# Kernel tuning notes

Hardware: AMD Instinct MI355X
Metric: run time of the kernel (lower is better)

The kernel has to match this reference:

```python
import jax, jax.numpy as jnp
import numpy as np

N = 200_000      # nodes
E = 6_400_000    # edges (avg degree 32)
IN = 128         # in_channels
H = 16           # GCN/GRU hidden size (fixed by module)
OUT = 32         # out_channels


def setup_inputs() -> dict:
    key = jax.random.key(0)
    ks = jax.random.split(key, 13)
    s = 0.1  # weight init scale
    return {
        "x": jax.random.normal(ks[0], (N, IN), jnp.float32),
        "edge_index": jax.random.randint(ks[1], (2, E), 0, N, dtype=jnp.int32),
        "batch": jnp.zeros((N,), jnp.int32),
        "W1": jax.random.normal(ks[2], (IN, H), jnp.float32) * s,
        "b1": jax.random.normal(ks[3], (H,), jnp.float32) * s,
        "W2": jax.random.normal(ks[4], (H, H), jnp.float32) * s,
        "b2": jax.random.normal(ks[5], (H,), jnp.float32) * s,
        # GRU params, torch layout: [3H, in] stacked (r, z, n)
        "w_ih": jax.random.normal(ks[6], (3 * H, H), jnp.float32) * s,
        "w_hh": jax.random.normal(ks[7], (3 * H, H), jnp.float32) * s,
        "b_ih": jax.random.normal(ks[8], (3 * H,), jnp.float32) * s,
        "b_hh": jax.random.normal(ks[9], (3 * H,), jnp.float32) * s,
        # final Linear
        "Wfc": jax.random.normal(ks[10], (OUT, H), jnp.float32) * s,
        "bfc": jax.random.normal(ks[11], (OUT,), jnp.float32) * s,
    }


def gcn_conv(x, edge_index, W, b):
    """PyG GCNConv: transform, then sym-normalized aggregate with self-loops."""
    n = x.shape[0]
    h = x @ W                                   # [N, H]
    src, dst = edge_index[0], edge_index[1]
    # degree with self-loops: 1 + in-degree at target nodes
    deg = jax.ops.segment_sum(jnp.ones_like(dst, jnp.float32), dst, num_segments=n) + 1.0
    dinv = jax.lax.rsqrt(deg)                   # [N]
    norm = dinv[src] * dinv[dst]                # [E]
    agg = jax.ops.segment_sum(h[src] * norm[:, None], dst, num_segments=n)
    # self-loop message: h[i] * dinv[i]^2
    agg = agg + h * (dinv * dinv)[:, None]
    return agg + b


def reference(x, edge_index, batch, W1, b1, W2, b2, w_ih, w_hh, b_ih, b_hh, Wfc, bfc):
    h = jax.nn.relu(gcn_conv(x, edge_index, W1, b1))
    h = jax.nn.relu(gcn_conv(h, edge_index, W2, b2))
    # x.view(batch.size(0), -1, 16) -> [N, 1, 16]: GRU with seq_len=1, h0=0
    n_nodes = batch.shape[0]
    h0 = jnp.zeros((n_nodes, H), h.dtype)
    gi = h @ w_ih.T + b_ih                      # [N, 3H]
    gh = h0 @ w_hh.T + b_hh                     # [N, 3H]
    i_r, i_z, i_n = jnp.split(gi, 3, axis=1)
    h_r, h_z, h_n = jnp.split(gh, 3, axis=1)
    r = jax.nn.sigmoid(i_r + h_r)
    z = jax.nn.sigmoid(i_z + h_z)
    n_ = jnp.tanh(i_n + r * h_n)
    hseq = (1.0 - z) * n_ + z * h0              # last (only) timestep output
    return hseq @ Wfc.T + bfc                   # [N, OUT]
```

## Files before the change

### kernel.cpp

```cpp
#include <hip/hip_runtime.h>
#include <hip/hip_fp16.h>
#include <math.h>

#define HC 16
#define INC 128
#define OUTC 32
#define BKT_SHIFT 8
#define CAP 9216
#define NBMAX 1024
#define BINS 12512

typedef _Float16 f16;
typedef _Float16 f16x8 __attribute__((ext_vector_type(8)));


__global__ void init_gcur_kernel(int* __restrict__ gcur, int nbkt) {
    int i = blockIdx.x * blockDim.x + threadIdx.x;
    if (i < nbkt) gcur[i] = i * CAP;
}

__global__ void __launch_bounds__(512) bin_kernel(
        const int* __restrict__ src, const int* __restrict__ dst,
        int* __restrict__ gcur, int* __restrict__ csrbuf, int e, int nbkt) {
    __shared__ int ent[BINS];
    __shared__ int hist[NBMAX];
    __shared__ int off[NBMAX];
    __shared__ int gbase[NBMAX];
    __shared__ int wsum[8];
    int tid = threadIdx.x;
    int beg = blockIdx.x * BINS;
    int end = min(beg + BINS, e);
    int sz = end - beg;
    if (sz <= 0) return;

    for (int i = tid; i < NBMAX; i += 512) hist[i] = 0;
    __syncthreads();
    for (int i = beg + tid; i < end; i += 512)
        atomicAdd(&hist[dst[i] >> BKT_SHIFT], 1);
    __syncthreads();
    int b0 = tid * 2;
    int c0 = hist[b0], c1 = hist[b0 + 1];
    int tsum = c0 + c1;
    int lane = tid & 63, wid = tid >> 6;
    int v = tsum;
#pragma unroll
    for (int d = 1; d < 64; d <<= 1) {
        int u = __shfl_up(v, d, 64);
        if (lane >= d) v += u;
    }
    if (lane == 63) wsum[wid] = v;
    __syncthreads();
    int wbase = 0;
#pragma unroll
    for (int w = 0; w < 8; ++w) wbase += (w < wid) ? wsum[w] : 0;
    int ex = wbase + v - tsum;
    off[b0]     = ex;
    off[b0 + 1] = ex + c0;
    if (c0) gbase[b0]     = atomicAdd(&gcur[b0], c0);
    if (c1) gbase[b0 + 1] = atomicAdd(&gcur[b0 + 1], c1);
    hist[b0] = 0; hist[b0 + 1] = 0;
    __syncthreads();
    for (int i = beg + tid; i < end; i += 512) {
        int d = dst[i];
        int b = d >> BKT_SHIFT;
        int p = off[b] + atomicAdd(&hist[b], 1);
        ent[p] = (src[i] & 0x3FFFF) | ((d & 255) << 18);
    }
    __syncthreads();
    for (int k0 = 0; k0 < sz; k0 += 512) {
        int k = k0 + tid;
        if (k < sz) {
            int lo = 0, hi = nbkt - 1;
            while (lo < hi) {
                int mid = (lo + hi + 1) >> 1;
                if (off[mid] <= k) lo = mid; else hi = mid - 1;
            }
            csrbuf[gbase[lo] + (k - off[lo])] = ent[k];
        }
    }
}

__global__ void __launch_bounds__(512) bucketize_kernel(
        const int* __restrict__ gcur, int* __restrict__ csrbuf,
        int* __restrict__ row_beg, int* __restrict__ row_end,
        float* __restrict__ dinv, int n) {
    __shared__ int ent[CAP];
    __shared__ int cnt[256];
    __shared__ int off[256];
    __shared__ int cur[256];
    int tid = threadIdx.x;
    int b = blockIdx.x;
    int base = b * CAP;
    int sz = gcur[b] - base;
    if (sz > CAP) sz = CAP;
    int node0 = b << BKT_SHIFT;
    int nnodes = min(256, n - node0);
    for (int i = tid; i < sz; i += 512) ent[i] = csrbuf[base + i];
    if (tid < 256) cnt[tid] = 0;
    __syncthreads();
    for (int i = tid; i < sz; i += 512) atomicAdd(&cnt[ent[i] >> 18], 1);
    __syncthreads();
    int v = (tid < 256) ? cnt[tid] : 0;
    if (tid < 256) off[tid] = v;
    __syncthreads();
    for (int d = 1; d < 256; d <<= 1) {
        int u = (tid < 256 && tid >= d) ? off[tid - d] : 0;
        __syncthreads();
        if (tid < 256) off[tid] += u;
        __syncthreads();
    }
    if (tid < 256) {
        int excl = off[tid] - v;
        cur[tid] = excl;
        if (tid < nnodes) {
            row_beg[node0 + tid] = base + excl;
            row_end[node0 + tid] = base + excl + v;
            dinv[node0 + tid] = rsqrtf((float)v + 1.0f);
        }
    }
    __syncthreads();
    for (int i = tid; i < sz; i += 512) {
        int p = ent[i];
        int dl = p >> 18;
        int pos = atomicAdd(&cur[dl], 1);
        csrbuf[base + pos] = p & 0x3FFFF;
    }
}

__global__ void gemm1_kernel(const float* __restrict__ x, const float* __restrict__ W1,
                             const float* __restrict__ dinv, f16* __restrict__ hd1, int n) {
    __shared__ float sW[INC * HC];
    for (int i = threadIdx.x; i < INC * HC; i += blockDim.x) sW[i] = W1[i];
    __syncthreads();
    int node = blockIdx.x * blockDim.x + threadIdx.x;
    if (node >= n) return;
    const float4* xr = (const float4*)(x + (size_t)node * INC);
    float acc[HC];
#pragma unroll
    for (int f = 0; f < HC; ++f) acc[f] = 0.f;
#pragma unroll 4
    for (int k4 = 0; k4 < INC / 4; ++k4) {
        float4 v = xr[k4];
        const float* w = &sW[k4 * 4 * HC];
#pragma unroll
        for (int f = 0; f < HC; ++f)
            acc[f] += v.x * w[f] + v.y * w[HC + f] + v.z * w[2 * HC + f] + v.w * w[3 * HC + f];
    }
    float di = dinv[node];
    union { f16 h[HC]; float4 q[2]; } u;
#pragma unroll
    for (int f = 0; f < HC; ++f) u.h[f] = (f16)(acc[f] * di);
    float4* hl = (float4*)(hd1 + (size_t)node * HC);
    hl[0] = u.q[0];
    hl[1] = u.q[1];
}

__device__ __forceinline__ float gather_row16(
        const f16* __restrict__ hd, const int* __restrict__ csr,
        int beg, int end, int node, int f) {
    int h = f & 1;
    int k = f >> 1;
    float a0 = 0.f, a1 = 0.f, a2 = 0.f, a3 = 0.f;
    float a4 = 0.f, a5 = 0.f, a6 = 0.f, a7 = 0.f;
    int jj = beg + k;
    if (jj < end) {
        int s = csr[jj];
        jj += 8;
        for (; jj < end; jj += 8) {
            int sn = csr[jj];
            f16x8 v = *(const f16x8*)(hd + ((size_t)s << 4) + (h << 3));
            a0 += (float)v[0]; a1 += (float)v[1]; a2 += (float)v[2]; a3 += (float)v[3];
            a4 += (float)v[4]; a5 += (float)v[5]; a6 += (float)v[6]; a7 += (float)v[7];
            s = sn;
        }
        f16x8 v = *(const f16x8*)(hd + ((size_t)s << 4) + (h << 3));
        a0 += (float)v[0]; a1 += (float)v[1]; a2 += (float)v[2]; a3 += (float)v[3];
        a4 += (float)v[4]; a5 += (float)v[5]; a6 += (float)v[6]; a7 += (float)v[7];
    }
#pragma unroll
    for (int m = 2; m <= 8; m <<= 1) {
        a0 += __shfl_xor(a0, m, 16); a1 += __shfl_xor(a1, m, 16);
        a2 += __shfl_xor(a2, m, 16); a3 += __shfl_xor(a3, m, 16);
        a4 += __shfl_xor(a4, m, 16); a5 += __shfl_xor(a5, m, 16);
        a6 += __shfl_xor(a6, m, 16); a7 += __shfl_xor(a7, m, 16);
    }
    float e = a0;
    e = (k == 1) ? a1 : e;
    e = (k == 2) ? a2 : e;
    e = (k == 3) ? a3 : e;
    e = (k == 4) ? a4 : e;
    e = (k == 5) ? a5 : e;
    e = (k == 6) ? a6 : e;
    e = (k == 7) ? a7 : e;
    float gsum = __shfl(e, ((f & 7) << 1) | (f >> 3), 16);
    return gsum + (float)hd[(size_t)node * HC + f];
}

__global__ void __launch_bounds__(256) gather_fuse1_kernel(
        const f16* __restrict__ hd1, const int* __restrict__ csr,
        const int* __restrict__ row_beg, const int* __restrict__ row_end,
        const float* __restrict__ dinv, const float* __restrict__ b1,
        const float* __restrict__ W2, f16* __restrict__ hd2, int n) {
    __shared__ float sW[HC * 17];
    __shared__ float sb[HC];
    if (threadIdx.x < HC * HC) sW[(threadIdx.x >> 4) * 17 + (threadIdx.x & 15)] = W2[threadIdx.x];
    if (threadIdx.x < HC) sb[threadIdx.x] = b1[threadIdx.x];
    __syncthreads();
    int t = blockIdx.x * blockDim.x + threadIdx.x;
    int node = t >> 4;
    if (node >= n) return;
    int f = t & 15;
    float acc = gather_row16(hd1, csr, row_beg[node], row_end[node], node, f);
    float di = dinv[node];
    float h1 = fmaxf(acc * di + sb[f], 0.f);
    float a2 = 0.f;
#pragma unroll
    for (int k = 0; k < HC; ++k) {
        float hk = __shfl(h1, k, 16);
        a2 += hk * sW[k * 17 + f];
    }
    hd2[(size_t)node * HC + f] = (f16)(a2 * di);
}

__global__ void __launch_bounds__(256) gather_final_kernel(
        const f16* __restrict__ hd2, const int* __restrict__ csr,
        const int* __restrict__ row_beg, const int* __restrict__ row_end,
        const float* __restrict__ dinv, const float* __restrict__ b2,
        const float* __restrict__ w_ih, const float* __restrict__ b_ih,
        const float* __restrict__ b_hh, const float* __restrict__ Wfc,
        const float* __restrict__ bfc, float* __restrict__ out, int n) {
    __shared__ float s_wih[3 * HC * 17];
    __shared__ float s_wfc[OUTC * 17];
    __shared__ float s_bih[3 * HC], s_bhh[3 * HC], s_bfc[OUTC], s_b2[HC];
    for (int i = threadIdx.x; i < 3 * HC * HC; i += 256)
        s_wih[(i >> 4) * 17 + (i & 15)] = w_ih[i];
    for (int i = threadIdx.x; i < OUTC * HC; i += 256)
        s_wfc[(i >> 4) * 17 + (i & 15)] = Wfc[i];
    if (threadIdx.x < 3 * HC) { s_bih[threadIdx.x] = b_ih[threadIdx.x]; s_bhh[threadIdx.x] = b_hh[threadIdx.x]; }
    if (threadIdx.x < OUTC) s_bfc[threadIdx.x] = bfc[threadIdx.x];
    if (threadIdx.x < HC) s_b2[threadIdx.x] = b2[threadIdx.x];
    __syncthreads();
    int t = blockIdx.x * blockDim.x + threadIdx.x;
    int node = t >> 4;
    if (node >= n) return;
    int f = t & 15;
    float acc = gather_row16(hd2, csr, row_beg[node], row_end[node], node, f);
    float h = fmaxf(acc * dinv[node] + s_b2[f], 0.f);
    float ir = s_bih[f], iz = s_bih[HC + f], inn = s_bih[2 * HC + f];
#pragma unroll
    for (int k = 0; k < HC; ++k) {
        float hk = __shfl(h, k, 16);
        ir  += hk * s_wih[f * 17 + k];
        iz  += hk * s_wih[(HC + f) * 17 + k];
        inn += hk * s_wih[(2 * HC + f) * 17 + k];
    }
    float r = 1.f / (1.f + __expf(-(ir + s_bhh[f])));
    float z = 1.f / (1.f + __expf(-(iz + s_bhh[HC + f])));
    float nn = tanhf(inn + r * s_bhh[2 * HC + f]);
    float hs = (1.f - z) * nn;
    float a1 = s_bfc[f], a2 = s_bfc[HC + f];
#pragma unroll
    for (int k = 0; k < HC; ++k) {
        float hk = __shfl(hs, k, 16);
        a1 += hk * s_wfc[f * 17 + k];
        a2 += hk * s_wfc[(HC + f) * 17 + k];
    }
    float* orow = out + (size_t)node * OUTC;
    __builtin_nontemporal_store(a1, orow + f);
    __builtin_nontemporal_store(a2, orow + HC + f);
}

extern "C" void kernel_launch(void* const* d_in, const int* in_sizes, int n_in,
                              void* d_out, int out_size, void* d_ws, size_t ws_size,
                              hipStream_t stream) {
    const float* x     = (const float*)d_in[0];
    const int*   ei    = (const int*)d_in[1];
    const float* W1    = (const float*)d_in[3];
    const float* b1    = (const float*)d_in[4];
    const float* W2    = (const float*)d_in[5];
    const float* b2    = (const float*)d_in[6];
    const float* w_ih  = (const float*)d_in[7];
    const float* b_ih  = (const float*)d_in[9];
    const float* b_hh  = (const float*)d_in[10];
    const float* Wfc   = (const float*)d_in[11];
    const float* bfc   = (const float*)d_in[12];
    float* out = (float*)d_out;

    const int n = in_sizes[2];
    const int e = in_sizes[1] / 2;
    const int* src = ei;
    const int* dst = ei + e;
    const int nbkt = (n + 255) >> BKT_SHIFT;

    int*   gcur    = (int*)d_ws;
    int*   row_beg = gcur + 1024;
    int*   row_end = row_beg + n;
    float* dinv    = (float*)(row_end + n);
    int*   csrbuf  = (int*)(dinv + n);
    f16*   hd1     = (f16*)(csrbuf + (size_t)nbkt * CAP);
    f16*   hd2     = hd1 + (size_t)n * HC;

    const int B = 256;
    int gn   = (n + B - 1) / B;
    int gnf  = (int)(((long long)n * HC + B - 1) / B);
    int gbin = (e + BINS - 1) / BINS;

    init_gcur_kernel<<<(NBMAX + B - 1) / B, B, 0, stream>>>(gcur, nbkt);
    bin_kernel<<<gbin, 512, 0, stream>>>(src, dst, gcur, csrbuf, e, nbkt);
    bucketize_kernel<<<nbkt, 512, 0, stream>>>(gcur, csrbuf, row_beg, row_end, dinv, n);

    gemm1_kernel<<<gn, B, 0, stream>>>(x, W1, dinv, hd1, n);
    gather_fuse1_kernel<<<gnf, B, 0, stream>>>(hd1, csrbuf, row_beg, row_end, dinv, b1, W2, hd2, n);
    gather_final_kernel<<<gnf, B, 0, stream>>>(hd2, csrbuf, row_beg, row_end, dinv, b2,
                                               w_ih, b_ih, b_hh, Wfc, bfc, out, n);
}
```

Measured before the change: 458.9 us.

## Cache edges in registers, copy bins per bucket, shuffle-scan in bucketize

New measurement: 448.2 us. 1.02x faster.

```diff
diff --git a/kernel.cpp b/kernel.cpp
--- a/kernel.cpp
+++ b/kernel.cpp
@@ -8,7 +8,8 @@
 #define BKT_SHIFT 8
 #define CAP 9216
 #define NBMAX 1024
-#define BINS 12512
+#define BINS 12288
+#define EPT 24
 
 typedef _Float16 f16;
 typedef _Float16 f16x8 __attribute__((ext_vector_type(8)));
@@ -30,14 +31,22 @@
     int tid = threadIdx.x;
     int beg = blockIdx.x * BINS;
     int end = min(beg + BINS, e);
-    int sz = end - beg;
-    if (sz <= 0) return;
-
+    if (end <= beg) return;
+
+    int myd[EPT], mys[EPT];
+#pragma unroll
+    for (int u = 0; u < EPT; ++u) {
+        int i = beg + u * 512 + tid;
+        myd[u] = (i < end) ? dst[i] : -1;
+        mys[u] = (i < end) ? src[i] : 0;
+    }
     for (int i = tid; i < NBMAX; i += 512) hist[i] = 0;
     __syncthreads();
-    for (int i = beg + tid; i < end; i += 512)
-        atomicAdd(&hist[dst[i] >> BKT_SHIFT], 1);
-    __syncthreads();
+#pragma unroll
+    for (int u = 0; u < EPT; ++u)
+        if (myd[u] >= 0) atomicAdd(&hist[myd[u] >> BKT_SHIFT], 1);
+    __syncthreads();
+
     int b0 = tid * 2;
     int c0 = hist[b0], c1 = hist[b0 + 1];
     int tsum = c0 + c1;
@@ -60,23 +69,27 @@
     if (c1) gbase[b0 + 1] = atomicAdd(&gcur[b0 + 1], c1);
     hist[b0] = 0; hist[b0 + 1] = 0;
     __syncthreads();
-    for (int i = beg + tid; i < end; i += 512) {
-        int d = dst[i];
-        int b = d >> BKT_SHIFT;
-        int p = off[b] + atomicAdd(&hist[b], 1);
-        ent[p] = (src[i] & 0x3FFFF) | ((d & 255) << 18);
-    }
-    __syncthreads();
-    for (int k0 = 0; k0 < sz; k0 += 512) {
-        int k = k0 + tid;
-        if (k < sz) {
-            int lo = 0, hi = nbkt - 1;
-            while (lo < hi) {
-                int mid = (lo + hi + 1) >> 1;
-                if (off[mid] <= k) lo = mid; else hi = mid - 1;
-            }
-            csrbuf[gbase[lo] + (k - off[lo])] = ent[k];
+
+#pragma unroll
+    for (int u = 0; u < EPT; ++u) {
+        int d = myd[u];
+        if (d >= 0) {
+            int b = d >> BKT_SHIFT;
+            int p = off[b] + atomicAdd(&hist[b], 1);
+            ent[p] = (mys[u] & 0x3FFFF) | ((d & 255) << 18);
         }
+    }
+    __syncthreads();
+
+    int grp = tid >> 4;
+    int gl  = tid & 15;
+    for (int b = grp; b < nbkt; b += 32) {
+        int o = off[b];
+        int c = off[b + 1] - o;
+        if (c <= 0) continue;
+        int g = gbase[b];
+        for (int k = gl; k < c; k += 16)
+            csrbuf[g + k] = ent[o + k];
     }
 }
 
@@ -88,6 +101,7 @@
     __shared__ int cnt[256];
     __shared__ int off[256];
     __shared__ int cur[256];
+    __shared__ int wsum2[4];
     int tid = threadIdx.x;
     int b = blockIdx.x;
     int base = b * CAP;
@@ -101,16 +115,21 @@
     for (int i = tid; i < sz; i += 512) atomicAdd(&cnt[ent[i] >> 18], 1);
     __syncthreads();
     int v = (tid < 256) ? cnt[tid] : 0;
-    if (tid < 256) off[tid] = v;
-    __syncthreads();
-    for (int d = 1; d < 256; d <<= 1) {
-        int u = (tid < 256 && tid >= d) ? off[tid - d] : 0;
-        __syncthreads();
-        if (tid < 256) off[tid] += u;
-        __syncthreads();
-    }
+    int lane = tid & 63, w = tid >> 6;
+    int vv = v;
+#pragma unroll
+    for (int d = 1; d < 64; d <<= 1) {
+        int u = __shfl_up(vv, d, 64);
+        if (lane >= d) vv += u;
+    }
+    if (tid < 256 && lane == 63) wsum2[w] = vv;
+    __syncthreads();
     if (tid < 256) {
-        int excl = off[tid] - v;
+        int wb = 0;
+#pragma unroll
+        for (int w2 = 0; w2 < 4; ++w2) wb += (w2 < w) ? wsum2[w2] : 0;
+        int incl = wb + vv;
+        int excl = incl - v;
         cur[tid] = excl;
         if (tid < nnodes) {
             row_beg[node0 + tid] = base + excl;
```

## Build CSR with global degree atomics and atomic scatter, fuse scan into GEMM1

Applied to the files above, without the earlier changes.

After: 1.127 ms. 146% more time.

```diff
diff --git a/kernel.cpp b/kernel.cpp
--- a/kernel.cpp
+++ b/kernel.cpp
@@ -7,132 +7,59 @@
 #define OUTC 32
 #define BKT_SHIFT 8
 #define CAP 9216
-#define NBMAX 1024
-#define BINS 12512
 
 typedef _Float16 f16;
 typedef _Float16 f16x8 __attribute__((ext_vector_type(8)));
 
 
-__global__ void init_gcur_kernel(int* __restrict__ gcur, int nbkt) {
-    int i = blockIdx.x * blockDim.x + threadIdx.x;
-    if (i < nbkt) gcur[i] = i * CAP;
-}
-
-__global__ void __launch_bounds__(512) bin_kernel(
-        const int* __restrict__ src, const int* __restrict__ dst,
-        int* __restrict__ gcur, int* __restrict__ csrbuf, int e, int nbkt) {
-    __shared__ int ent[BINS];
-    __shared__ int hist[NBMAX];
-    __shared__ int off[NBMAX];
-    __shared__ int gbase[NBMAX];
-    __shared__ int wsum[8];
+__global__ void __launch_bounds__(256) degree_kernel(
+        const int* __restrict__ dst, int* __restrict__ deg, int e) {
+    int q = blockIdx.x * blockDim.x + threadIdx.x;
+    int j = q * 4;
+    if (j + 3 < e) {
+        int4 d4 = *(const int4*)(dst + j);
+        atomicAdd(&deg[d4.x], 1);
+        atomicAdd(&deg[d4.y], 1);
+        atomicAdd(&deg[d4.z], 1);
+        atomicAdd(&deg[d4.w], 1);
+    } else {
+        for (; j < e; ++j) atomicAdd(&deg[dst[j]], 1);
+    }
+}
+
+__global__ void __launch_bounds__(256) scan_gemm_kernel(
+        const int* __restrict__ deg, const float* __restrict__ x,
+        const float* __restrict__ W1, int* __restrict__ row_beg,
+        int* __restrict__ row_end, float* __restrict__ dinv,
+        f16* __restrict__ hd1, int n) {
+    __shared__ float sW[INC * HC];
+    __shared__ int wsum2[4];
     int tid = threadIdx.x;
-    int beg = blockIdx.x * BINS;
-    int end = min(beg + BINS, e);
-    int sz = end - beg;
-    if (sz <= 0) return;
-
-    for (int i = tid; i < NBMAX; i += 512) hist[i] = 0;
-    __syncthreads();
-    for (int i = beg + tid; i < end; i += 512)
-        atomicAdd(&hist[dst[i] >> BKT_SHIFT], 1);
-    __syncthreads();
-    int b0 = tid * 2;
-    int c0 = hist[b0], c1 = hist[b0 + 1];
-    int tsum = c0 + c1;
-    int lane = tid & 63, wid = tid >> 6;
-    int v = tsum;
-#pragma unroll
-    for (int d = 1; d < 64; d <<= 1) {
-        int u = __shfl_up(v, d, 64);
-        if (lane >= d) v += u;
-    }
-    if (lane == 63) wsum[wid] = v;
-    __syncthreads();
-    int wbase = 0;
-#pragma unroll
-    for (int w = 0; w < 8; ++w) wbase += (w < wid) ? wsum[w] : 0;
-    int ex = wbase + v - tsum;
-    off[b0]     = ex;
-    off[b0 + 1] = ex + c0;
-    if (c0) gbase[b0]     = atomicAdd(&gcur[b0], c0);
-    if (c1) gbase[b0 + 1] = atomicAdd(&gcur[b0 + 1], c1);
-    hist[b0] = 0; hist[b0 + 1] = 0;
-    __syncthreads();
-    for (int i = beg + tid; i < end; i += 512) {
-        int d = dst[i];
-        int b = d >> BKT_SHIFT;
-        int p = off[b] + atomicAdd(&hist[b], 1);
-        ent[p] = (src[i] & 0x3FFFF) | ((d & 255) << 18);
-    }
-    __syncthreads();
-    for (int k0 = 0; k0 < sz; k0 += 512) {
-        int k = k0 + tid;
-        if (k < sz) {
-            int lo = 0, hi = nbkt - 1;
-            while (lo < hi) {
-                int mid = (lo + hi + 1) >> 1;
-                if (off[mid] <= k) lo = mid; else hi = mid - 1;
-            }
-            csrbuf[gbase[lo] + (k - off[lo])] = ent[k];
-        }
-    }
-}
-
-__global__ void __launch_bounds__(512) bucketize_kernel(
-        const int* __restrict__ gcur, int* __restrict__ csrbuf,
-        int* __restrict__ row_beg, int* __restrict__ row_end,
-        float* __restrict__ dinv, int n) {
-    __shared__ int ent[CAP];
-    __shared__ int cnt[256];
-    __shared__ int off[256];
-    __shared__ int cur[256];
-    int tid = threadIdx.x;
-    int b = blockIdx.x;
-    int base = b * CAP;
-    int sz = gcur[b] - base;
-    if (sz > CAP) sz = CAP;
-    int node0 = b << BKT_SHIFT;
-    int nnodes = min(256, n - node0);
-    for (int i = tid; i < sz; i += 512) ent[i] = csrbuf[base + i];
-    if (tid < 256) cnt[tid] = 0;
-    __syncthreads();
-    for (int i = tid; i < sz; i += 512) atomicAdd(&cnt[ent[i] >> 18], 1);
-    __syncthreads();
-    int v = (tid < 256) ? cnt[tid] : 0;
-    if (tid < 256) off[tid] = v;
-    __syncthreads();
-    for (int d = 1; d < 256; d <<= 1) {
-        int u = (tid < 256 && tid >= d) ? off[tid - d] : 0;
-        __syncthreads();
-        if (tid < 256) off[tid] += u;
-        __syncthreads();
-    }
-    if (tid < 256) {
-        int excl = off[tid] - v;
-        cur[tid] = excl;
-        if (tid < nnodes) {
-            row_beg[node0 + tid] = base + excl;
-            row_end[node0 + tid] = base + excl + v;
-            dinv[node0 + tid] = rsqrtf((float)v + 1.0f);
-        }
-    }
-    __syncthreads();
-    for (int i = tid; i < sz; i += 512) {
-        int p = ent[i];
-        int dl = p >> 18;
-        int pos = atomicAdd(&cur[dl], 1);
-        csrbuf[base + pos] = p & 0x3FFFF;
-    }
-}
-
-__global__ void gemm1_kernel(const float* __restrict__ x, const float* __restrict__ W1,
-                             const float* __restrict__ dinv, f16* __restrict__ hd1, int n) {
-    __shared__ float sW[INC * HC];
-    for (int i = threadIdx.x; i < INC * HC; i += blockDim.x) sW[i] = W1[i];
-    __syncthreads();
-    int node = blockIdx.x * blockDim.x + threadIdx.x;
+    int node0 = blockIdx.x << BKT_SHIFT;
+    int node = node0 + tid;
+    int d = (node < n) ? deg[node] : 0;
+    int lane = tid & 63, w = tid >> 6;
+    int vv = d;
+#pragma unroll
+    for (int s = 1; s < 64; s <<= 1) {
+        int u = __shfl_up(vv, s, 64);
+        if (lane >= s) vv += u;
+    }
+    if (lane == 63) wsum2[w] = vv;
+    __syncthreads();
+    int wb = 0;
+#pragma unroll
+    for (int w2 = 0; w2 < 4; ++w2) wb += (w2 < w) ? wsum2[w2] : 0;
+    int excl = wb + vv - d;
+    int base = blockIdx.x * CAP;
+    float di = rsqrtf((float)d + 1.0f);
+    if (node < n) {
+        row_beg[node] = base + excl;
+        row_end[node] = base + excl;
+        dinv[node] = di;
+    }
+    for (int i = tid; i < INC * HC; i += 256) sW[i] = W1[i];
+    __syncthreads();
     if (node >= n) return;
     const float4* xr = (const float4*)(x + (size_t)node * INC);
     float acc[HC];
@@ -141,18 +68,41 @@
 #pragma unroll 4
     for (int k4 = 0; k4 < INC / 4; ++k4) {
         float4 v = xr[k4];
-        const float* w = &sW[k4 * 4 * HC];
+        const float* wp = &sW[k4 * 4 * HC];
 #pragma unroll
         for (int f = 0; f < HC; ++f)
-            acc[f] += v.x * w[f] + v.y * w[HC + f] + v.z * w[2 * HC + f] + v.w * w[3 * HC + f];
-    }
-    float di = dinv[node];
+            acc[f] += v.x * wp[f] + v.y * wp[HC + f] + v.z * wp[2 * HC + f] + v.w * wp[3 * HC + f];
+    }
     union { f16 h[HC]; float4 q[2]; } u;
 #pragma unroll
     for (int f = 0; f < HC; ++f) u.h[f] = (f16)(acc[f] * di);
     float4* hl = (float4*)(hd1 + (size_t)node * HC);
     hl[0] = u.q[0];
     hl[1] = u.q[1];
+}
+
+__global__ void __launch_bounds__(256) scatter_kernel(
+        const int* __restrict__ src, const int* __restrict__ dst,
+        int* __restrict__ row_end, int* __restrict__ csrbuf, int e) {
+    int q = blockIdx.x * blockDim.x + threadIdx.x;
+    int j = q * 4;
+    if (j + 3 < e) {
+        int4 s4 = *(const int4*)(src + j);
+        int4 d4 = *(const int4*)(dst + j);
+        int p0 = atomicAdd(&row_end[d4.x], 1);
+        int p1 = atomicAdd(&row_end[d4.y], 1);
+        int p2 = atomicAdd(&row_end[d4.z], 1);
+        int p3 = atomicAdd(&row_end[d4.w], 1);
+        csrbuf[p0] = s4.x;
+        csrbuf[p1] = s4.y;
+        csrbuf[p2] = s4.z;
+        csrbuf[p3] = s4.w;
+    } else {
+        for (; j < e; ++j) {
+            int p = atomicAdd(&row_end[dst[j]], 1);
+            csrbuf[p] = src[j];
+        }
+    }
 }
 
 __device__ __forceinline__ float gather_row16(
@@ -292,8 +242,8 @@
     const int* dst = ei + e;
     const int nbkt = (n + 255) >> BKT_SHIFT;
 
-    int*   gcur    = (int*)d_ws;
-    int*   row_beg = gcur + 1024;
+    int*   deg     = (int*)d_ws;
+    int*   row_beg = deg + n;
     int*   row_end = row_beg + n;
     float* dinv    = (float*)(row_end + n);
     int*   csrbuf  = (int*)(dinv + n);
@@ -301,15 +251,13 @@
     f16*   hd2     = hd1 + (size_t)n * HC;
 
     const int B = 256;
-    int gn   = (n + B - 1) / B;
-    int gnf  = (int)(((long long)n * HC + B - 1) / B);
-    int gbin = (e + BINS - 1) / BINS;
-
-    init_gcur_kernel<<<(NBMAX + B - 1) / B, B, 0, stream>>>(gcur, nbkt);
-    bin_kernel<<<gbin, 512, 0, stream>>>(src, dst, gcur, csrbuf, e, nbkt);
-    bucketize_kernel<<<nbkt, 512, 0, stream>>>(gcur, csrbuf, row_beg, row_end, dinv, n);
-
-    gemm1_kernel<<<gn, B, 0, stream>>>(x, W1, dinv, hd1, n);
+    int gnf = (int)(((long long)n * HC + B - 1) / B);
+    int gq  = (e / 4 + B - 1) / B;
+
+    hipMemsetAsync(deg, 0, (size_t)n * sizeof(int), stream);
+    degree_kernel<<<gq, B, 0, stream>>>(dst, deg, e);
+    scan_gemm_kernel<<<nbkt, B, 0, stream>>>(deg, x, W1, row_beg, row_end, dinv, hd1, n);
+    scatter_kernel<<<gq, B, 0, stream>>>(src, dst, row_end, csrbuf, e);
     gather_fuse1_kernel<<<gnf, B, 0, stream>>>(hd1, csrbuf, row_beg, row_end, dinv, b1, W2, hd2, n);
     gather_final_kernel<<<gnf, B, 0, stream>>>(hd2, csrbuf, row_beg, row_end, dinv, b2,
                                                w_ih, b_ih, b_hh, Wfc, bfc, out, n);
```
